# Kernel tuning notes

Measured on AMD Instinct MI355X. Metric: run time of the kernel, lower is better.

## Reference

```python
import jax, jax.numpy as jnp
import numpy as np

B, L, D = 2, 2048, 1024
H, G = 16, 2            # num_heads, num_kv_groups
HPG = H // G            # heads per kv group = 8
DQK, DV = 128, 128      # qk_head_dim, v_head_dim (head_dim=64, ratios=2.0)


def setup_inputs() -> dict:
    key = jax.random.key(0)
    ks = jax.random.split(key, 12)

    def xavier(k, shape, scale=1.0):
        fan_in, fan_out = shape[0], shape[1]
        lim = np.sqrt(6.0 / (fan_in + fan_out))
        return jax.random.uniform(k, shape, jnp.float32, -lim, lim) * scale

    return {
        "in_q": jax.random.normal(ks[0], (B, L, D), jnp.float32),
        "in_k": jax.random.normal(ks[1], (B, L, D), jnp.float32),
        "in_v": jax.random.normal(ks[2], (B, L, D), jnp.float32),
        # weights stored as [in, out] (transpose of torch Linear); qk_init_scale=0.5
        "Wq": xavier(ks[3], (D, H * DQK), 0.5),
        "bq": jnp.zeros((H * DQK,), jnp.float32),
        "Wk": xavier(ks[4], (D, G * DQK), 0.5),
        "bk": jnp.zeros((G * DQK,), jnp.float32),
        "Wv": xavier(ks[5], (D, G * DV)),
        "bv": jnp.zeros((G * DV,), jnp.float32),
        "Wo": xavier(ks[6], (H * DV, D)),
        "bo": jnp.zeros((D,), jnp.float32),
        "q_extra_scale": jnp.ones((1,), jnp.float32),
    }


def reference(in_q, in_k, in_v, Wq, bq, Wk, bk, Wv, bv, Wo, bo, q_extra_scale):
    # fused projections
    q = (in_q @ Wq + bq) * q_extra_scale              # [B,L,H*DQK]
    k = in_k @ Wk + bk                                 # [B,L,G*DQK]
    v = in_v @ Wv + bv                                 # [B,L,G*DV]

    # reshape: keep GQA group structure instead of materializing repeat_interleave
    q = q.reshape(B, L, G, HPG, DQK)                   # heads grouped: head h = g*HPG + m
    k = k.reshape(B, L, G, DQK)
    v = v.reshape(B, L, G, DV)

    scale = 1.0 / np.sqrt(DQK)
    # scores: [B,G,HPG,L_q,L_kv]
    scores = jnp.einsum("bsgmd,btgd->bgmst", q, k) * scale
    causal = jnp.tril(jnp.ones((L, L), bool))          # is_causal=True
    scores = jnp.where(causal, scores, jnp.finfo(scores.dtype).min)
    attn = jax.nn.softmax(scores, axis=-1)
    ctx = jnp.einsum("bgmst,btgd->bsgmd", attn, v)     # [B,L,G,HPG,DV]
    ctx = ctx.reshape(B, L, H * DV)
    return ctx @ Wo + bo                               # [B,L,D]
```

## Files before the change

### kernel.cpp

```cpp
#include <hip/hip_runtime.h>


typedef __bf16 bf16;
typedef __bf16 bf16x8 __attribute__((ext_vector_type(8)));
typedef __bf16 bf16x4 __attribute__((ext_vector_type(4)));
typedef float f32x4 __attribute__((ext_vector_type(4)));
typedef float float4v __attribute__((ext_vector_type(4)));

#define MFMA_BF16(a, b, c) __builtin_amdgcn_mfma_f32_16x16x32_bf16((a), (b), (c), 0, 0, 0)

static constexpr int Bz = 2, Lz = 2048, Dz = 1024;
static constexpr int Hz = 16, Gz = 2;
static constexpr int DQKz = 128, DVz = 128;

__device__ __forceinline__ void async_copy16(const bf16* g, bf16* l) {
    __builtin_amdgcn_global_load_lds(
        (const __attribute__((address_space(1))) unsigned int*)g,
        (__attribute__((address_space(3))) unsigned int*)l, 16, 0, 0);
}

__global__ __launch_bounds__(256) void prep(
    const float* __restrict__ q, const float* __restrict__ k,
    const float* __restrict__ v, bf16* __restrict__ dq,
    bf16* __restrict__ dk, bf16* __restrict__ dv,
    const float* __restrict__ Wq, const float* __restrict__ Wk,
    const float* __restrict__ Wv, const float* __restrict__ Wo,
    bf16* __restrict__ WqT, bf16* __restrict__ WkT,
    bf16* __restrict__ WvT, bf16* __restrict__ WoT)
{
    int bid = blockIdx.x;
    if (bid < 6144) {
        const float* s = bid < 2048 ? q : (bid < 4096 ? k : v);
        bf16* d = bid < 2048 ? dq : (bid < 4096 ? dk : dv);
        int i = (bid & 2047) * 2048 + threadIdx.x * 8;
        float4v a = *(const float4v*)(s + i);
        float4v b = *(const float4v*)(s + i + 4);
        bf16x8 o;
        #pragma unroll
        for (int j = 0; j < 4; ++j) { o[j] = (bf16)a[j]; o[j + 4] = (bf16)b[j]; }
        *(bf16x8*)(d + i) = o;
        return;
    }
    bid -= 6144;
    const float* W; bf16* WT; int K, N;
    if (bid < 2048)      { W = Wq; WT = WqT; K = 1024; N = 2048; }
    else if (bid < 2304) { W = Wk; WT = WkT; K = 1024; N = 256;  bid -= 2048; }
    else if (bid < 2560) { W = Wv; WT = WvT; K = 1024; N = 256;  bid -= 2304; }
    else                 { W = Wo; WT = WoT; K = 2048; N = 1024; bid -= 2560; }
    int tiles_n = N >> 5;
    int n0 = (bid % tiles_n) * 32, k0 = (bid / tiles_n) * 32;

    __shared__ bf16 t[32][33];
    int tx = threadIdx.x & 31, ty = threadIdx.x >> 5;
    #pragma unroll
    for (int i = 0; i < 4; ++i)
        t[ty + i * 8][tx] = (bf16)W[(size_t)(k0 + ty + i * 8) * N + n0 + tx];
    __syncthreads();
    #pragma unroll
    for (int i = 0; i < 4; ++i)
        WT[(size_t)(n0 + ty + i * 8) * K + k0 + tx] = t[tx][ty + i * 8];
}

template <typename TC>
__device__ __forceinline__ void gemm_tile(
    const bf16* __restrict__ A, const bf16* __restrict__ BT,
    const float* __restrict__ bias, float scale, TC* __restrict__ C,
    int M, int N, int K, int m0, int n0, bool trans_out,
    bf16 (&As)[2][128 * 64], bf16 (&Bs)[2][128 * 64])
{
    const int tid  = threadIdx.x;
    const int wave = tid >> 6;
    const int lane = tid & 63;
    const int quad = lane >> 4;
    const int l16  = lane & 15;
    const int sw   = l16 & 7;
    const int wm = wave >> 2, wn = wave & 3;

    f32x4 acc[4][2] = {};

    auto stage = [&](int k0, int buf) {
        #pragma unroll
        for (int s = 0; s < 2; ++s) {
            int i = s * 512 + tid;
            int row = i >> 3, c = (i & 7) ^ (row & 7);
            async_copy16(A + (size_t)(m0 + row) * K + k0 + c * 8, &As[buf][i * 8]);
        }
        #pragma unroll
        for (int s = 0; s < 2; ++s) {
            int i = s * 512 + tid;
            int row = i >> 3, c = (i & 7) ^ (row & 7);
            async_copy16(BT + (size_t)(n0 + row) * K + k0 + c * 8, &Bs[buf][i * 8]);
        }
    };

    stage(0, 0);
    int cur = 0;
    for (int k0 = 0; k0 < K; k0 += 64) {
        __syncthreads();
        if (k0 + 64 < K) stage(k0 + 64, cur ^ 1);

        #pragma unroll
        for (int ks = 0; ks < 2; ++ks) {
            bf16x8 af[4], bfv[2];
            #pragma unroll
            for (int mt = 0; mt < 4; ++mt)
                af[mt] = *(const bf16x8*)(&As[cur][((wm * 64 + mt * 16 + l16) * 8
                                                    + ((ks * 4 + quad) ^ sw)) * 8]);
            #pragma unroll
            for (int nt = 0; nt < 2; ++nt)
                bfv[nt] = *(const bf16x8*)(&Bs[cur][((wn * 32 + nt * 16 + l16) * 8
                                                     + ((ks * 4 + quad) ^ sw)) * 8]);
            #pragma unroll
            for (int mt = 0; mt < 4; ++mt)
                #pragma unroll
                for (int nt = 0; nt < 2; ++nt)
                    acc[mt][nt] = MFMA_BF16(af[mt], bfv[nt], acc[mt][nt]);
        }
        cur ^= 1;
    }

    #pragma unroll
    for (int nt = 0; nt < 2; ++nt) {
        int col = n0 + wn * 32 + nt * 16 + l16;
        float bv = bias[col];
        #pragma unroll
        for (int mt = 0; mt < 4; ++mt) {
            int row = m0 + wm * 64 + mt * 16 + quad * 4;
            if (trans_out) {
                struct V4 { TC v[4]; } o;
                #pragma unroll
                for (int r = 0; r < 4; ++r)
                    o.v[r] = (TC)((acc[mt][nt][r] + bv) * scale);
                *(V4*)(&C[(size_t)col * M + row]) = o;
            } else {
                #pragma unroll
                for (int r = 0; r < 4; ++r)
                    C[(size_t)(row + r) * N + col] =
                        (TC)((acc[mt][nt][r] + bv) * scale);
            }
        }
    }
}

__global__ __launch_bounds__(512, 4) void proj_qkv(
    const bf16* __restrict__ aq, const bf16* __restrict__ ak,
    const bf16* __restrict__ av, const bf16* __restrict__ WqT,
    const bf16* __restrict__ WkT, const bf16* __restrict__ WvT,
    const float* __restrict__ bq, const float* __restrict__ bk,
    const float* __restrict__ bv, const float* __restrict__ qsc,
    bf16* __restrict__ Qw, bf16* __restrict__ Kw, bf16* __restrict__ VwT)
{
    __shared__ bf16 As[2][128 * 64];
    __shared__ bf16 Bs[2][128 * 64];
    int bid = blockIdx.x;
    if (bid < 512) {
        int xcd = bid & 7, rest = bid >> 3;
        int n = rest & 15, mg = rest >> 4;
        int m = mg * 8 + xcd;
        float scale = qsc[0] * 0.08838834764831845f * 1.4426950408889634f;
        gemm_tile<bf16>(aq, WqT, bq, scale, Qw, 4096, 2048, 1024,
                        m * 128, n * 128, false, As, Bs);
    } else if (bid < 576) {
        int b2 = bid - 512;
        gemm_tile<bf16>(ak, WkT, bk, 1.0f, Kw, 4096, 256, 1024,
                        (b2 >> 1) * 128, (b2 & 1) * 128, false, As, Bs);
    } else {
        int b2 = bid - 576;
        gemm_tile<bf16>(av, WvT, bv, 1.0f, VwT, 4096, 256, 1024,
                        (b2 >> 1) * 128, (b2 & 1) * 128, true, As, Bs);
    }
}

__global__ __launch_bounds__(512, 4) void proj_o(
    const bf16* __restrict__ Cw, const bf16* __restrict__ WoT,
    const float* __restrict__ bo, float* __restrict__ out)
{
    __shared__ bf16 As[2][128 * 64];
    __shared__ bf16 Bs[2][128 * 64];
    int xcd = blockIdx.x & 7, rest = blockIdx.x >> 3;
    int n = rest & 7, mg = rest >> 3;
    int m = mg * 8 + xcd;
    gemm_tile<float>(Cw, WoT, bo, 1.0f, out, 4096, 1024, 2048,
                     m * 128, n * 128, false, As, Bs);
}

__global__ __launch_bounds__(512, 4) void attn_fused(
    const bf16* __restrict__ Q,
    const bf16* __restrict__ Kp,
    const bf16* __restrict__ VT,
    bf16* __restrict__ ctx)
{
    __shared__ bf16 Kb[2][64 * 128];
    __shared__ bf16 Vb[2][128 * 64];
    __shared__ bf16 Ps[8][16 * 64];

    const int tid  = threadIdx.x;
    const int wave = tid >> 6;
    const int lane = tid & 63;
    const int quad = lane >> 4;
    const int l16  = lane & 15;
    const int sw   = l16 & 7;

    const int gph = blockIdx.y;
    const int g   = gph >> 1;
    const int h   = g * 8 + (gph & 1) * 4 + (wave >> 1);
    const int b   = blockIdx.z;
    const int wrow = wave & 1;

    const bf16* kgbase = Kp + (size_t)(b * Lz) * (Gz * DQKz) + g * DQKz;
    const bf16* vgbase = VT + (size_t)(g * DVz) * (Bz * Lz) + b * Lz;

    auto stage = [&](int kt, int buf) {
        const bf16* kb = kgbase + (size_t)(kt * 64) * (Gz * DQKz);
        #pragma unroll
        for (int s = 0; s < 2; ++s) {
            int i = s * 512 + tid;
            int key = i >> 4, c = (i & 15) ^ (key & 7);
            async_copy16(kb + (size_t)key * (Gz * DQKz) + c * 8, &Kb[buf][i * 8]);
        }
        const bf16* vb = vgbase + kt * 64;
        #pragma unroll
        for (int s = 0; s < 2; ++s) {
            int i = s * 512 + tid;
            int dv = i >> 3, c = (i & 7) ^ (dv & 7);
            async_copy16(vb + (size_t)dv * (Bz * Lz) + c * 8, &Vb[buf][i * 8]);
        }
    };

    bf16* ps = Ps[wave];

    for (int pass = 0; pass < 2; ++pass) {
        const int qt  = pass == 0 ? (63 - blockIdx.x) : blockIdx.x;
        const int q0  = qt * 32;
        const int nkt = (qt >> 1) + 1;
        const int qrow = q0 + wrow * 16 + l16;

        bf16x8 qf[4];
        {
            const bf16* qbase = Q + (size_t)(b * Lz + qrow) * (Hz * DQKz) + h * DQKz;
            #pragma unroll
            for (int ks = 0; ks < 4; ++ks)
                qf[ks] = *(const bf16x8*)(qbase + ks * 32 + quad * 8);
        }

        f32x4 oacc[8] = {};
        float lsum = 0.0f;

        if (pass) __syncthreads();
        stage(0, 0);
        int cur = 0;

        for (int kt = 0; kt < nkt; ++kt) {
            __syncthreads();
            if (kt + 1 < nkt) stage(kt + 1, cur ^ 1);

            const bf16* kcur = Kb[cur];
            const bf16* vcur = Vb[cur];

            f32x4 sacc[4] = {};
            #pragma unroll
            for (int nf = 0; nf < 4; ++nf) {
                #pragma unroll
                for (int ks = 0; ks < 4; ++ks) {
                    bf16x8 kf = *(const bf16x8*)(&kcur[((nf * 16 + l16) * 16
                                                        + ((ks * 4 + quad) ^ sw)) * 8]);
                    sacc[nf] = MFMA_BF16(kf, qf[ks], sacc[nf]);
                }
            }

            float pv[4][4];
            if (kt == nkt - 1) {
                const int kv0 = kt * 64;
                #pragma unroll
                for (int nf = 0; nf < 4; ++nf) {
                    int keyb = kv0 + nf * 16 + quad * 4;
                    #pragma unroll
                    for (int r = 0; r < 4; ++r)
                        pv[nf][r] = (keyb + r > qrow) ? 0.0f
                                                      : exp2f(sacc[nf][r] - 8.0f);
                }
            } else {
                #pragma unroll
                for (int nf = 0; nf < 4; ++nf)
                    #pragma unroll
                    for (int r = 0; r < 4; ++r)
                        pv[nf][r] = exp2f(sacc[nf][r] - 8.0f);
            }

            #pragma unroll
            for (int nf = 0; nf < 4; ++nf)
                lsum += (pv[nf][0] + pv[nf][1]) + (pv[nf][2] + pv[nf][3]);

            #pragma unroll
            for (int nf = 0; nf < 4; ++nf) {
                bf16x4 pk;
                #pragma unroll
                for (int r = 0; r < 4; ++r) pk[r] = (bf16)pv[nf][r];
                int c16 = nf * 2 + (quad >> 1);
                *(bf16x4*)(&ps[l16 * 64 + ((c16 ^ sw) << 3) + ((quad & 1) << 2)]) = pk;
            }

            #pragma unroll
            for (int ks2 = 0; ks2 < 2; ++ks2) {
                bf16x8 pf = *(const bf16x8*)(&ps[l16 * 64
                                                 + (((ks2 * 4 + quad) ^ sw) << 3)]);
                #pragma unroll
                for (int nf2 = 0; nf2 < 8; ++nf2) {
                    bf16x8 vf = *(const bf16x8*)(&vcur[((nf2 * 16 + l16) * 8
                                                        + ((ks2 * 4 + quad) ^ sw)) * 8]);
                    oacc[nf2] = MFMA_BF16(vf, pf, oacc[nf2]);
                }
            }
            cur ^= 1;
        }

        lsum += __shfl_xor(lsum, 16);
        lsum += __shfl_xor(lsum, 32);
        const float inv = 1.0f / lsum;

        bf16* cbase = ctx + (size_t)(b * Lz + qrow) * (Hz * DVz) + h * DVz;
        #pragma unroll
        for (int nf2 = 0; nf2 < 8; ++nf2) {
            bf16x4 o4;
            #pragma unroll
            for (int r = 0; r < 4; ++r) o4[r] = (bf16)(oacc[nf2][r] * inv);
            *(bf16x4*)(&cbase[nf2 * 16 + quad * 4]) = o4;
        }
    }
}

extern "C" void kernel_launch(void* const* d_in, const int* in_sizes, int n_in,
                              void* d_out, int out_size, void* d_ws, size_t ws_size,
                              hipStream_t stream)
{
    (void)in_sizes; (void)n_in; (void)out_size; (void)ws_size;

    const float* in_q = (const float*)d_in[0];
    const float* in_k = (const float*)d_in[1];
    const float* in_v = (const float*)d_in[2];
    const float* Wq   = (const float*)d_in[3];
    const float* bq   = (const float*)d_in[4];
    const float* Wk   = (const float*)d_in[5];
    const float* bk   = (const float*)d_in[6];
    const float* Wv   = (const float*)d_in[7];
    const float* bv   = (const float*)d_in[8];
    const float* Wo   = (const float*)d_in[9];
    const float* bo   = (const float*)d_in[10];
    const float* qsc  = (const float*)d_in[11];
    float* out = (float*)d_out;

    const int M = Bz * Lz;

    bf16* aq  = (bf16*)d_ws;
    bf16* WqT = aq  + (size_t)M * Dz;
    bf16* WkT = WqT + (size_t)2048 * 1024;
    bf16* WvT = WkT + (size_t)256 * 1024;
    bf16* WoT = WvT + (size_t)256 * 1024;
    bf16* Qw  = WoT + (size_t)1024 * 2048;
    bf16* Kw  = Qw  + (size_t)M * 2048;
    bf16* VwT = Kw  + (size_t)M * 256;
    bf16* Cw  = VwT + (size_t)256 * M;
    bf16* ak  = Cw;
    bf16* av  = Cw + (size_t)M * Dz;

    prep<<<dim3(10752), dim3(256), 0, stream>>>(
        in_q, in_k, in_v, aq, ak, av, Wq, Wk, Wv, Wo, WqT, WkT, WvT, WoT);

    proj_qkv<<<dim3(640), dim3(512), 0, stream>>>(
        aq, ak, av, WqT, WkT, WvT, bq, bk, bv, qsc, Qw, Kw, VwT);

    attn_fused<<<dim3(32, 4, 2), dim3(512), 0, stream>>>(Qw, Kw, VwT, Cw);

    proj_o<<<dim3(256), dim3(512), 0, stream>>>(Cw, WoT, bo, out);
}
```

Measured before the change: 260.4 us.

## Use 4-wave GEMM tiles for QKV projection and split attention passes into separate blocks

The QKV projection now runs 256-thread blocks where each wave computes a 64x64 sub-tile (4x4 MFMA fragments) instead of 512 threads with 64x32 sub-tiles. This raises register reuse per wave and lowers the wave count per block. The attention kernel no longer has each block do two causal passes (a long and a short query tile). It launches 512 one-pass blocks with a flattened index that interleaves batch and head-group and schedules the long tiles first. This gives more blocks for load balance across CUs, at the cost of losing the paired-pass balancing within a block and adding more registers per thread in the GEMM.

```diff
diff --git a/kernel.cpp b/kernel.cpp
--- a/kernel.cpp
+++ b/kernel.cpp
@@ -62,10 +62,91 @@
 }
 
 template <typename TC>
-__device__ __forceinline__ void gemm_tile(
+__device__ __forceinline__ void gemm_tile4(
     const bf16* __restrict__ A, const bf16* __restrict__ BT,
     const float* __restrict__ bias, float scale, TC* __restrict__ C,
     int M, int N, int K, int m0, int n0, bool trans_out,
+    bf16 (&As)[2][128 * 64], bf16 (&Bs)[2][128 * 64])
+{
+    const int tid  = threadIdx.x;
+    const int wave = tid >> 6;
+    const int lane = tid & 63;
+    const int quad = lane >> 4;
+    const int l16  = lane & 15;
+    const int sw   = l16 & 7;
+    const int wm = wave >> 1, wn = wave & 1;
+
+    f32x4 acc[4][4] = {};
+
+    auto stage = [&](int k0, int buf) {
+        #pragma unroll
+        for (int s = 0; s < 4; ++s) {
+            int i = s * 256 + tid;
+            int row = i >> 3, c = (i & 7) ^ (row & 7);
+            async_copy16(A + (size_t)(m0 + row) * K + k0 + c * 8, &As[buf][i * 8]);
+        }
+        #pragma unroll
+        for (int s = 0; s < 4; ++s) {
+            int i = s * 256 + tid;
+            int row = i >> 3, c = (i & 7) ^ (row & 7);
+            async_copy16(BT + (size_t)(n0 + row) * K + k0 + c * 8, &Bs[buf][i * 8]);
+        }
+    };
+
+    stage(0, 0);
+    int cur = 0;
+    for (int k0 = 0; k0 < K; k0 += 64) {
+        __syncthreads();
+        if (k0 + 64 < K) stage(k0 + 64, cur ^ 1);
+
+        #pragma unroll
+        for (int ks = 0; ks < 2; ++ks) {
+            bf16x8 af[4], bfv[4];
+            #pragma unroll
+            for (int mt = 0; mt < 4; ++mt)
+                af[mt] = *(const bf16x8*)(&As[cur][((wm * 64 + mt * 16 + l16) * 8
+                                                    + ((ks * 4 + quad) ^ sw)) * 8]);
+            #pragma unroll
+            for (int nt = 0; nt < 4; ++nt)
+                bfv[nt] = *(const bf16x8*)(&Bs[cur][((wn * 64 + nt * 16 + l16) * 8
+                                                     + ((ks * 4 + quad) ^ sw)) * 8]);
+            #pragma unroll
+            for (int mt = 0; mt < 4; ++mt)
+                #pragma unroll
+                for (int nt = 0; nt < 4; ++nt)
+                    acc[mt][nt] = MFMA_BF16(af[mt], bfv[nt], acc[mt][nt]);
+        }
+        cur ^= 1;
+    }
+
+    #pragma unroll
+    for (int nt = 0; nt < 4; ++nt) {
+        int col = n0 + wn * 64 + nt * 16 + l16;
+        float bv = bias[col];
+        #pragma unroll
+        for (int mt = 0; mt < 4; ++mt) {
+            int row = m0 + wm * 64 + mt * 16 + quad * 4;
+            if (trans_out) {
+                struct V4 { TC v[4]; } o;
+                #pragma unroll
+                for (int r = 0; r < 4; ++r)
+                    o.v[r] = (TC)((acc[mt][nt][r] + bv) * scale);
+                *(V4*)(&C[(size_t)col * M + row]) = o;
+            } else {
+                #pragma unroll
+                for (int r = 0; r < 4; ++r)
+                    C[(size_t)(row + r) * N + col] =
+                        (TC)((acc[mt][nt][r] + bv) * scale);
+            }
+        }
+    }
+}
+
+template <typename TC>
+__device__ __forceinline__ void gemm_tile8(
+    const bf16* __restrict__ A, const bf16* __restrict__ BT,
+    const float* __restrict__ bias, float scale, TC* __restrict__ C,
+    int M, int N, int K, int m0, int n0,
     bf16 (&As)[2][128 * 64], bf16 (&Bs)[2][128 * 64])
 {
     const int tid  = threadIdx.x;
@@ -126,23 +207,14 @@
         #pragma unroll
         for (int mt = 0; mt < 4; ++mt) {
             int row = m0 + wm * 64 + mt * 16 + quad * 4;
-            if (trans_out) {
-                struct V4 { TC v[4]; } o;
-                #pragma unroll
-                for (int r = 0; r < 4; ++r)
-                    o.v[r] = (TC)((acc[mt][nt][r] + bv) * scale);
-                *(V4*)(&C[(size_t)col * M + row]) = o;
-            } else {
-                #pragma unroll
-                for (int r = 0; r < 4; ++r)
-                    C[(size_t)(row + r) * N + col] =
-                        (TC)((acc[mt][nt][r] + bv) * scale);
-            }
-        }
-    }
-}
-
-__global__ __launch_bounds__(512, 4) void proj_qkv(
+            #pragma unroll
+            for (int r = 0; r < 4; ++r)
+                C[(size_t)(row + r) * N + col] = (TC)((acc[mt][nt][r] + bv) * scale);
+        }
+    }
+}
+
+__global__ __launch_bounds__(256, 2) void proj_qkv(
     const bf16* __restrict__ aq, const bf16* __restrict__ ak,
     const bf16* __restrict__ av, const bf16* __restrict__ WqT,
     const bf16* __restrict__ WkT, const bf16* __restrict__ WvT,
@@ -158,16 +230,16 @@
         int n = rest & 15, mg = rest >> 4;
         int m = mg * 8 + xcd;
         float scale = qsc[0] * 0.08838834764831845f * 1.4426950408889634f;
-        gemm_tile<bf16>(aq, WqT, bq, scale, Qw, 4096, 2048, 1024,
-                        m * 128, n * 128, false, As, Bs);
+        gemm_tile4<bf16>(aq, WqT, bq, scale, Qw, 4096, 2048, 1024,
+                         m * 128, n * 128, false, As, Bs);
     } else if (bid < 576) {
         int b2 = bid - 512;
-        gemm_tile<bf16>(ak, WkT, bk, 1.0f, Kw, 4096, 256, 1024,
-                        (b2 >> 1) * 128, (b2 & 1) * 128, false, As, Bs);
+        gemm_tile4<bf16>(ak, WkT, bk, 1.0f, Kw, 4096, 256, 1024,
+                         (b2 >> 1) * 128, (b2 & 1) * 128, false, As, Bs);
     } else {
         int b2 = bid - 576;
-        gemm_tile<bf16>(av, WvT, bv, 1.0f, VwT, 4096, 256, 1024,
-                        (b2 >> 1) * 128, (b2 & 1) * 128, true, As, Bs);
+        gemm_tile4<bf16>(av, WvT, bv, 1.0f, VwT, 4096, 256, 1024,
+                         (b2 >> 1) * 128, (b2 & 1) * 128, true, As, Bs);
     }
 }
 
@@ -180,8 +252,8 @@
     int xcd = blockIdx.x & 7, rest = blockIdx.x >> 3;
     int n = rest & 7, mg = rest >> 3;
     int m = mg * 8 + xcd;
-    gemm_tile<float>(Cw, WoT, bo, 1.0f, out, 4096, 1024, 2048,
-                     m * 128, n * 128, false, As, Bs);
+    gemm_tile8<float>(Cw, WoT, bo, 1.0f, out, 4096, 1024, 2048,
+                      m * 128, n * 128, As, Bs);
 }
 
 __global__ __launch_bounds__(512, 4) void attn_fused(
@@ -201,11 +273,21 @@
     const int l16  = lane & 15;
     const int sw   = l16 & 7;
 
-    const int gph = blockIdx.y;
-    const int g   = gph >> 1;
-    const int h   = g * 8 + (gph & 1) * 4 + (wave >> 1);
-    const int b   = blockIdx.z;
+    const int bid  = blockIdx.x;
+    const int half = bid >> 8;
+    const int rem  = bid & 255;
+    const int gph  = (rem & 7) >> 1;
+    const int b    = rem & 1;
+    const int p    = rem >> 3;
+    const int qt   = half ? p : (63 - p);
+
+    const int g    = gph >> 1;
+    const int h    = g * 8 + (gph & 1) * 4 + (wave >> 1);
     const int wrow = wave & 1;
+
+    const int q0  = qt * 32;
+    const int nkt = (qt >> 1) + 1;
+    const int qrow = q0 + wrow * 16 + l16;
 
     const bf16* kgbase = Kp + (size_t)(b * Lz) * (Gz * DQKz) + g * DQKz;
     const bf16* vgbase = VT + (size_t)(g * DVz) * (Bz * Lz) + b * Lz;
@@ -229,103 +311,95 @@
 
     bf16* ps = Ps[wave];
 
-    for (int pass = 0; pass < 2; ++pass) {
-        const int qt  = pass == 0 ? (63 - blockIdx.x) : blockIdx.x;
-        const int q0  = qt * 32;
-        const int nkt = (qt >> 1) + 1;
-        const int qrow = q0 + wrow * 16 + l16;
-
-        bf16x8 qf[4];
-        {
-            const bf16* qbase = Q + (size_t)(b * Lz + qrow) * (Hz * DQKz) + h * DQKz;
-            #pragma unroll
-            for (int ks = 0; ks < 4; ++ks)
-                qf[ks] = *(const bf16x8*)(qbase + ks * 32 + quad * 8);
-        }
-
-        f32x4 oacc[8] = {};
-        float lsum = 0.0f;
-
-        if (pass) __syncthreads();
-        stage(0, 0);
-        int cur = 0;
-
-        for (int kt = 0; kt < nkt; ++kt) {
-            __syncthreads();
-            if (kt + 1 < nkt) stage(kt + 1, cur ^ 1);
-
-            const bf16* kcur = Kb[cur];
-            const bf16* vcur = Vb[cur];
-
-            f32x4 sacc[4] = {};
+    bf16x8 qf[4];
+    {
+        const bf16* qbase = Q + (size_t)(b * Lz + qrow) * (Hz * DQKz) + h * DQKz;
+        #pragma unroll
+        for (int ks = 0; ks < 4; ++ks)
+            qf[ks] = *(const bf16x8*)(qbase + ks * 32 + quad * 8);
+    }
+
+    f32x4 oacc[8] = {};
+    float lsum = 0.0f;
+
+    stage(0, 0);
+    int cur = 0;
+
+    for (int kt = 0; kt < nkt; ++kt) {
+        __syncthreads();
+        if (kt + 1 < nkt) stage(kt + 1, cur ^ 1);
+
+        const bf16* kcur = Kb[cur];
+        const bf16* vcur = Vb[cur];
+
+        f32x4 sacc[4] = {};
+        #pragma unroll
+        for (int nf = 0; nf < 4; ++nf) {
+            #pragma unroll
+            for (int ks = 0; ks < 4; ++ks) {
+                bf16x8 kf = *(const bf16x8*)(&kcur[((nf * 16 + l16) * 16
+                                                    + ((ks * 4 + quad) ^ sw)) * 8]);
+                sacc[nf] = MFMA_BF16(kf, qf[ks], sacc[nf]);
+            }
+        }
+
+        float pv[4][4];
+        if (kt == nkt - 1) {
+            const int kv0 = kt * 64;
             #pragma unroll
             for (int nf = 0; nf < 4; ++nf) {
-                #pragma unroll
-                for (int ks = 0; ks < 4; ++ks) {
-                    bf16x8 kf = *(const bf16x8*)(&kcur[((nf * 16 + l16) * 16
-                                                        + ((ks * 4 + quad) ^ sw)) * 8]);
-                    sacc[nf] = MFMA_BF16(kf, qf[ks], sacc[nf]);
-                }
+                int keyb = kv0 + nf * 16 + quad * 4;
+                #pragma unroll
+                for (int r = 0; r < 4; ++r)
+                    pv[nf][r] = (keyb + r > qrow) ? 0.0f
+                                                  : exp2f(sacc[nf][r] - 8.0f);
             }
-
-            float pv[4][4];
-            if (kt == nkt - 1) {
-                const int kv0 = kt * 64;
-                #pragma unroll
-                for (int nf = 0; nf < 4; ++nf) {
-                    int keyb = kv0 + nf * 16 + quad * 4;
-                    #pragma unroll
-                    for (int r = 0; r < 4; ++r)
-                        pv[nf][r] = (keyb + r > qrow) ? 0.0f
-                                                      : exp2f(sacc[nf][r] - 8.0f);
-                }
-            } else {
-                #pragma unroll
-                for (int nf = 0; nf < 4; ++nf)
-                    #pragma unroll
-                    for (int r = 0; r < 4; ++r)
-                        pv[nf][r] = exp2f(sacc[nf][r] - 8.0f);
+        } else {
+            #pragma unroll
+            for (int nf = 0; nf < 4; ++nf)
+                #pragma unroll
+                for (int r = 0; r < 4; ++r)
+                    pv[nf][r] = exp2f(sacc[nf][r] - 8.0f);
+        }
+
+        #pragma unroll
+        for (int nf = 0; nf < 4; ++nf)
+            lsum += (pv[nf][0] + pv[nf][1]) + (pv[nf][2] + pv[nf][3]);
+
+        #pragma unroll
+        for (int nf = 0; nf < 4; ++nf) {
+            bf16x4 pk;
+            #pragma unroll
+            for (int r = 0; r < 4; ++r) pk[r] = (bf16)pv[nf][r];
+            int c16 = nf * 2 + (quad >> 1);
+            *(bf16x4*)(&ps[l16 * 64 + ((c16 ^ sw) << 3) + ((quad & 1) << 2)]) = pk;
+        }
+
+        #pragma unroll
+        for (int ks2 = 0; ks2 < 2; ++ks2) {
+            bf16x8 pf = *(const bf16x8*)(&ps[l16 * 64
+                                             + (((ks2 * 4 + quad) ^ sw) << 3)]);
+            #pragma unroll
+            for (int nf2 = 0; nf2 < 8; ++nf2) {
+                bf16x8 vf = *(const bf16x8*)(&vcur[((nf2 * 16 + l16) * 8
+                                                    + ((ks2 * 4 + quad) ^ sw)) * 8]);
+                oacc[nf2] = MFMA_BF16(vf, pf, oacc[nf2]);
             }
-
-            #pragma unroll
-            for (int nf = 0; nf < 4; ++nf)
-                lsum += (pv[nf][0] + pv[nf][1]) + (pv[nf][2] + pv[nf][3]);
-
-            #pragma unroll
-            for (int nf = 0; nf < 4; ++nf) {
-                bf16x4 pk;
-                #pragma unroll
-                for (int r = 0; r < 4; ++r) pk[r] = (bf16)pv[nf][r];
-                int c16 = nf * 2 + (quad >> 1);
-                *(bf16x4*)(&ps[l16 * 64 + ((c16 ^ sw) << 3) + ((quad & 1) << 2)]) = pk;
-            }
-
-            #pragma unroll
-            for (int ks2 = 0; ks2 < 2; ++ks2) {
-                bf16x8 pf = *(const bf16x8*)(&ps[l16 * 64
-                                                 + (((ks2 * 4 + quad) ^ sw) << 3)]);
-                #pragma unroll
-                for (int nf2 = 0; nf2 < 8; ++nf2) {
-                    bf16x8 vf = *(const bf16x8*)(&vcur[((nf2 * 16 + l16) * 8
-                                                        + ((ks2 * 4 + quad) ^ sw)) * 8]);
-                    oacc[nf2] = MFMA_BF16(vf, pf, oacc[nf2]);
-                }
-            }
-            cur ^= 1;
-        }
-
-        lsum += __shfl_xor(lsum, 16);
-        lsum += __shfl_xor(lsum, 32);
-        const float inv = 1.0f / lsum;
-
-        bf16* cbase = ctx + (size_t)(b * Lz + qrow) * (Hz * DVz) + h * DVz;
-        #pragma unroll
-        for (int nf2 = 0; nf2 < 8; ++nf2) {
-            bf16x4 o4;
-            #pragma unroll
-            for (int r = 0; r < 4; ++r) o4[r] = (bf16)(oacc[nf2][r] * inv);
-            *(bf16x4*)(&cbase[nf2 * 16 + quad * 4]) = o4;
-        }
+        }
+        cur ^= 1;
+    }
+
+    lsum += __shfl_xor(lsum, 16);
+    lsum += __shfl_xor(lsum, 32);
+    const float inv = 1.0f / lsum;
+
+    bf16* cbase = ctx + (size_t)(b * Lz + qrow) * (Hz * DVz) + h * DVz;
+    #pragma unroll
+    for (int nf2 = 0; nf2 < 8; ++nf2) {
+        bf16x4 o4;
+        #pragma unroll
+        for (int r = 0; r < 4; ++r) o4[r] = (bf16)(oacc[nf2][r] * inv);
+        *(bf16x4*)(&cbase[nf2 * 16 + quad * 4]) = o4;
     }
 }
 
@@ -366,10 +440,10 @@
     prep<<<dim3(10752), dim3(256), 0, stream>>>(
         in_q, in_k, in_v, aq, ak, av, Wq, Wk, Wv, Wo, WqT, WkT, WvT, WoT);
 
-    proj_qkv<<<dim3(640), dim3(512), 0, stream>>>(
+    proj_qkv<<<dim3(640), dim3(256), 0, stream>>>(
         aq, ak, av, WqT, WkT, WvT, bq, bk, bv, qsc, Qw, Kw, VwT);
 
-    attn_fused<<<dim3(32, 4, 2), dim3(512), 0, stream>>>(Qw, Kw, VwT, Cw);
+    attn_fused<<<dim3(512), dim3(512), 0, stream>>>(Qw, Kw, VwT, Cw);
 
     proj_o<<<dim3(256), dim3(512), 0, stream>>>(Cw, WoT, bo, out);
 }
```

Result: no change. 262.1 us (+0.7%).
